# Optimization experiments

Hardware: AMD Instinct MI355X
Metric: run time of the kernel (lower is better)

Reference implementation:

```python
import jax, jax.numpy as jnp
import numpy as np

NUM_NODES = 4096
EMBED_DIM = 64
IN_DIM = 256
OUT_DIM = 256
BATCH = 32


def setup_inputs() -> dict:
    key = jax.random.key(0)
    k1, k2, k3 = jax.random.split(key, 3)
    x = jax.random.normal(k1, (BATCH, NUM_NODES, IN_DIM), dtype=jnp.float32)
    node_ids = jnp.arange(NUM_NODES, dtype=jnp.int64)
    emb_table = jax.random.normal(k2, (NUM_NODES, EMBED_DIM), dtype=jnp.float32) * 0.1
    W = jax.random.normal(k3, (IN_DIM, OUT_DIM), dtype=jnp.float32) * (1.0 / np.sqrt(IN_DIM))
    b = jnp.zeros((OUT_DIM,), dtype=jnp.float32)
    return {"x": x, "node_ids": node_ids, "emb_table": emb_table, "W": W, "b": b}


def reference(x, node_ids, emb_table, W, b):
    # Embedding lookup for node ids -> [N, E]
    E = emb_table[node_ids]
    # Adaptive adjacency from embeddings: softmax(relu(E E^T)) over neighbors
    logits = jax.nn.relu(jnp.einsum("ne,me->nm", E, E))  # [N, N]
    adj = jax.nn.softmax(logits, axis=-1)
    # Graph convolution: aggregate neighbor features, then linear + relu
    h = jnp.einsum("nm,bmd->bnd", adj, x)          # [B, N, in_dim]
    out = jax.nn.relu(jnp.einsum("bnd,do->bno", h, W) + b)  # [B, N, out_dim]
    return out
```

## Files before the change

### kernel.cpp

```cpp
#include <hip/hip_runtime.h>

#define NN   4096
#define ED   64
#define DIN  256
#define DOUT 256
#define NB   32

typedef __attribute__((ext_vector_type(8))) short bf16x8;
typedef __attribute__((ext_vector_type(4))) float f32x4;

__device__ __forceinline__ unsigned short f2bf(float f) {
    union { float f; unsigned u; } v; v.f = f;
    unsigned r = v.u + 0x7FFF + ((v.u >> 16) & 1);
    return (unsigned short)(r >> 16);
}
__device__ __forceinline__ float bf2f(unsigned short s) {
    union { unsigned u; float f; } v; v.u = ((unsigned)s) << 16;
    return v.f;
}

#define GLDS16(g, l) __builtin_amdgcn_global_load_lds( \
    (const __attribute__((address_space(1))) void*)(g), \
    (__attribute__((address_space(3))) void*)(l), 16, 0, 0)

__device__ __forceinline__ void fma4(float4& d, float s, const float4& v) {
    d.x = fmaf(s, v.x, d.x);
    d.y = fmaf(s, v.y, d.y);
    d.z = fmaf(s, v.z, d.z);
    d.w = fmaf(s, v.w, d.w);
}

__global__ void k_gather(const float* __restrict__ emb, const int* __restrict__ ids,
                         float* __restrict__ E) {
    int n = blockIdx.x;
    int e = threadIdx.x;
    int id = ids[n];
    id = id < 0 ? 0 : (id >= NN ? NN - 1 : id);
    E[(size_t)n * ED + e] = emb[(size_t)id * ED + e];
}

__global__ __launch_bounds__(256) void k_logits(const float* __restrict__ E,
                                                unsigned short* __restrict__ adjbf) {
    __shared__ __align__(16) float Ea[ED][64 + 4];
    __shared__ __align__(16) float Eb[ED][64 + 4];
    const int tid = threadIdx.x;
    const int ty = tid >> 4, tx = tid & 15;
    const int rb = blockIdx.x, cb = blockIdx.y;

    #pragma unroll
    for (int k = 0; k < 4; ++k) {
        int l = tid + k * 256;
        int row = l >> 4;
        int kq = (l & 15) * 4;
        float4 va = *(const float4*)&E[(size_t)(rb * 64 + row) * ED + kq];
        Ea[kq + 0][row] = va.x; Ea[kq + 1][row] = va.y;
        Ea[kq + 2][row] = va.z; Ea[kq + 3][row] = va.w;
        float4 vb = *(const float4*)&E[(size_t)(cb * 64 + row) * ED + kq];
        Eb[kq + 0][row] = vb.x; Eb[kq + 1][row] = vb.y;
        Eb[kq + 2][row] = vb.z; Eb[kq + 3][row] = vb.w;
    }
    __syncthreads();

    float4 acc[4] = {};
    #pragma unroll
    for (int k = 0; k < ED; ++k) {
        float4 ar = *(const float4*)&Ea[k][ty * 4];
        float4 br = *(const float4*)&Eb[k][tx * 4];
        fma4(acc[0], ar.x, br);
        fma4(acc[1], ar.y, br);
        fma4(acc[2], ar.z, br);
        fma4(acc[3], ar.w, br);
    }

    #pragma unroll
    for (int i = 0; i < 4; ++i) {
        float4 v = acc[i];
        ushort4 s;
        s.x = f2bf(fmaxf(v.x, 0.f)); s.y = f2bf(fmaxf(v.y, 0.f));
        s.z = f2bf(fmaxf(v.z, 0.f)); s.w = f2bf(fmaxf(v.w, 0.f));
        size_t n = (size_t)(rb * 64 + ty * 4 + i);
        *(ushort4*)&adjbf[n * NN + cb * 64 + tx * 4] = s;
    }
}

__global__ __launch_bounds__(256) void k_softmax(unsigned short* __restrict__ adj) {
    __shared__ float red[256];
    const int tid = threadIdx.x;
    const size_t base = (size_t)blockIdx.x * NN + (size_t)tid * 16;

    unsigned short t16[16];
    *(uint4*)&t16[0] = *(const uint4*)&adj[base];
    *(uint4*)&t16[8] = *(const uint4*)&adj[base + 8];
    float v[16];
    float mx = 0.0f;
    #pragma unroll
    for (int j = 0; j < 16; ++j) { v[j] = bf2f(t16[j]); mx = fmaxf(mx, v[j]); }

    red[tid] = mx; __syncthreads();
    for (int off = 128; off > 0; off >>= 1) {
        if (tid < off) red[tid] = fmaxf(red[tid], red[tid + off]);
        __syncthreads();
    }
    mx = red[0];
    __syncthreads();

    float s = 0.f;
    #pragma unroll
    for (int j = 0; j < 16; ++j) { v[j] = expf(v[j] - mx); s += v[j]; }
    red[tid] = s; __syncthreads();
    for (int off = 128; off > 0; off >>= 1) {
        if (tid < off) red[tid] += red[tid + off];
        __syncthreads();
    }
    const float inv = 1.0f / red[0];

    #pragma unroll
    for (int j = 0; j < 16; ++j) t16[j] = f2bf(v[j] * inv);
    *(uint4*)&adj[base]     = *(const uint4*)&t16[0];
    *(uint4*)&adj[base + 8] = *(const uint4*)&t16[8];
}

__global__ void k_wt(const float* __restrict__ W, unsigned short* __restrict__ WT) {
    int m = blockIdx.x;
    int k = threadIdx.x;
    WT[(size_t)m * DIN + k] = f2bf(W[(size_t)k * DOUT + m]);
}

__global__ __launch_bounds__(256) void k_y(const unsigned short* __restrict__ WT,
                                           const float* __restrict__ x,
                                           unsigned short* __restrict__ yT) {
    __shared__ __align__(16) short As[128 * 32];
    __shared__ __align__(16) short Bs[128 * 32];
    const int tid = threadIdx.x;
    const int lane = tid & 63, w = tid >> 6;
    const int wr = (w >> 1) * 64, wc = (w & 1) * 64;
    const int fr = lane & 15, fq = lane >> 4;
    const int m0 = blockIdx.x * 128;
    const int n0 = blockIdx.y * 128;
    const int b  = blockIdx.z;
    const float* xb = x + (size_t)b * NN * DIN;
    const int brow = tid >> 1, bh = (tid & 1) * 16;

    f32x4 acc[4][4];
    #pragma unroll
    for (int i = 0; i < 4; ++i)
        #pragma unroll
        for (int j = 0; j < 4; ++j) acc[i][j] = (f32x4){0.f, 0.f, 0.f, 0.f};

    for (int k0 = 0; k0 < DIN; k0 += 32) {
        __syncthreads();
        #pragma unroll
        for (int i = 0; i < 2; ++i) {
            int idx = (w * 2 + i) * 512 + lane * 8;
            int row = idx >> 5, kk = idx & 31;
            GLDS16(WT + (size_t)(m0 + row) * DIN + k0 + kk, &As[(w * 2 + i) * 512]);
        }
        float fv[16];
        *(float4*)&fv[0]  = *(const float4*)&xb[(size_t)(n0 + brow) * DIN + k0 + bh + 0];
        *(float4*)&fv[4]  = *(const float4*)&xb[(size_t)(n0 + brow) * DIN + k0 + bh + 4];
        *(float4*)&fv[8]  = *(const float4*)&xb[(size_t)(n0 + brow) * DIN + k0 + bh + 8];
        *(float4*)&fv[12] = *(const float4*)&xb[(size_t)(n0 + brow) * DIN + k0 + bh + 12];
        unsigned u[8];
        #pragma unroll
        for (int j = 0; j < 8; ++j)
            u[j] = (unsigned)f2bf(fv[2 * j]) | ((unsigned)f2bf(fv[2 * j + 1]) << 16);
        *(uint4*)&Bs[brow * 32 + bh]     = make_uint4(u[0], u[1], u[2], u[3]);
        *(uint4*)&Bs[brow * 32 + bh + 8] = make_uint4(u[4], u[5], u[6], u[7]);
        __syncthreads();

        bf16x8 a[4], bb[4];
        #pragma unroll
        for (int mi = 0; mi < 4; ++mi)
            a[mi] = *(const bf16x8*)&As[(wr + mi * 16 + fr) * 32 + fq * 8];
        #pragma unroll
        for (int ni = 0; ni < 4; ++ni)
            bb[ni] = *(const bf16x8*)&Bs[(wc + ni * 16 + fr) * 32 + fq * 8];
        #pragma unroll
        for (int mi = 0; mi < 4; ++mi)
            #pragma unroll
            for (int ni = 0; ni < 4; ++ni)
                acc[mi][ni] = __builtin_amdgcn_mfma_f32_16x16x32_bf16(
                    a[mi], bb[ni], acc[mi][ni], 0, 0, 0);
    }

    unsigned short* yb = yT + (size_t)b * DOUT * NN;
    #pragma unroll
    for (int mi = 0; mi < 4; ++mi)
        #pragma unroll
        for (int ni = 0; ni < 4; ++ni)
            #pragma unroll
            for (int r = 0; r < 4; ++r) {
                int row = m0 + wr + mi * 16 + fq * 4 + r;
                int col = n0 + wc + ni * 16 + fr;
                yb[(size_t)row * NN + col] = f2bf(acc[mi][ni][r]);
            }
}

__global__ __launch_bounds__(512, 2) void k_gcn(const unsigned short* __restrict__ adj,
                                                const unsigned short* __restrict__ yT,
                                                const float* __restrict__ bias,
                                                float* __restrict__ out) {
    __shared__ __align__(16) char smem[131072];

    const int tid  = threadIdx.x;
    const int lane = tid & 63, wid = tid >> 6;
    const int fr = lane & 15, fq = lane >> 4;
    const int wr = wid >> 2, wc = wid & 3;
    const int m0 = blockIdx.x * 256;
    const int by = blockIdx.y;

    const char* Apanel = (const char*)(adj + (size_t)m0 * NN);
    const char* Bpanel = (const char*)(yT + (size_t)by * DOUT * NN);

    #define STAGE4(gpan, ktb, ldsb)                                              \
        {                                                                        \
            _Pragma("unroll")                                                    \
            for (int c = 0; c < 4; ++c) {                                        \
                int bo  = c * 8192 + wid * 1024 + lane * 16;                     \
                int row = bo >> 7;                                               \
                int scol = (bo & 127) ^ ((row & 7) << 4);                        \
                GLDS16((gpan) + (size_t)row * 8192 + (ktb) + scol,               \
                       (ldsb) + c * 8192 + wid * 1024);                          \
            }                                                                    \
        }

    STAGE4(Bpanel, 0,   smem + 32768);
    STAGE4(Apanel, 0,   smem);
    STAGE4(Bpanel, 128, smem + 65536 + 32768);
    STAGE4(Apanel, 128, smem + 65536);

    f32x4 acc[8][4];
    #pragma unroll
    for (int i = 0; i < 8; ++i)
        #pragma unroll
        for (int j = 0; j < 4; ++j) acc[i][j] = (f32x4){0.f, 0.f, 0.f, 0.f};

    const int xorp0 = (fq << 4) ^ ((fr & 7) << 4);
    const int xorp1 = (64 | (fq << 4)) ^ ((fr & 7) << 4);
    const int abase = (wr * 128 + fr) * 128;
    const int bbase = (wc * 64 + fr) * 128;

    bf16x8 Ar[4][2], Br[4][2];

    for (int j = 0; j < 64; ++j) {
        const int cur = j & 1;
        char* bufA = smem + cur * 65536;
        char* bufB = bufA + 32768;

        if (j + 1 < 64) { asm volatile("s_waitcnt vmcnt(8)" ::: "memory"); }
        else            { asm volatile("s_waitcnt vmcnt(0)" ::: "memory"); }
        __builtin_amdgcn_sched_barrier(0);
        __builtin_amdgcn_s_barrier();

        #pragma unroll
        for (int mi = 0; mi < 4; ++mi) {
            Ar[mi][0] = *(const bf16x8*)(bufA + abase + mi * 2048 + xorp0);
            Ar[mi][1] = *(const bf16x8*)(bufA + abase + mi * 2048 + xorp1);
        }
        #pragma unroll
        for (int ni = 0; ni < 2; ++ni) {
            Br[ni][0] = *(const bf16x8*)(bufB + bbase + ni * 2048 + xorp0);
            Br[ni][1] = *(const bf16x8*)(bufB + bbase + ni * 2048 + xorp1);
        }
        __builtin_amdgcn_s_barrier();
        asm volatile("s_waitcnt lgkmcnt(0)" ::: "memory");
        __builtin_amdgcn_sched_barrier(0);
        __builtin_amdgcn_s_setprio(1);
        #pragma unroll
        for (int mi = 0; mi < 4; ++mi)
            #pragma unroll
            for (int ni = 0; ni < 2; ++ni) {
                acc[mi][ni] = __builtin_amdgcn_mfma_f32_16x16x32_bf16(Ar[mi][0], Br[ni][0], acc[mi][ni], 0, 0, 0);
                acc[mi][ni] = __builtin_amdgcn_mfma_f32_16x16x32_bf16(Ar[mi][1], Br[ni][1], acc[mi][ni], 0, 0, 0);
            }
        __builtin_amdgcn_s_setprio(0);
        __builtin_amdgcn_s_barrier();

        #pragma unroll
        for (int ni = 2; ni < 4; ++ni) {
            Br[ni][0] = *(const bf16x8*)(bufB + bbase + ni * 2048 + xorp0);
            Br[ni][1] = *(const bf16x8*)(bufB + bbase + ni * 2048 + xorp1);
        }
        __builtin_amdgcn_s_barrier();
        asm volatile("s_waitcnt lgkmcnt(0)" ::: "memory");
        __builtin_amdgcn_sched_barrier(0);
        __builtin_amdgcn_s_setprio(1);
        #pragma unroll
        for (int mi = 0; mi < 4; ++mi)
            #pragma unroll
            for (int ni = 2; ni < 4; ++ni) {
                acc[mi][ni] = __builtin_amdgcn_mfma_f32_16x16x32_bf16(Ar[mi][0], Br[ni][0], acc[mi][ni], 0, 0, 0);
                acc[mi][ni] = __builtin_amdgcn_mfma_f32_16x16x32_bf16(Ar[mi][1], Br[ni][1], acc[mi][ni], 0, 0, 0);
            }
        __builtin_amdgcn_s_setprio(0);
        __builtin_amdgcn_s_barrier();

        #pragma unroll
        for (int mi = 0; mi < 4; ++mi) {
            Ar[mi][0] = *(const bf16x8*)(bufA + abase + 8192 + mi * 2048 + xorp0);
            Ar[mi][1] = *(const bf16x8*)(bufA + abase + 8192 + mi * 2048 + xorp1);
        }
        if (j + 2 < 64) STAGE4(Bpanel, (j + 2) * 128, bufB);
        __builtin_amdgcn_s_barrier();
        asm volatile("s_waitcnt lgkmcnt(0)" ::: "memory");
        __builtin_amdgcn_sched_barrier(0);
        __builtin_amdgcn_s_setprio(1);
        #pragma unroll
        for (int mi = 0; mi < 4; ++mi)
            #pragma unroll
            for (int ni = 0; ni < 2; ++ni) {
                acc[4 + mi][ni] = __builtin_amdgcn_mfma_f32_16x16x32_bf16(Ar[mi][0], Br[ni][0], acc[4 + mi][ni], 0, 0, 0);
                acc[4 + mi][ni] = __builtin_amdgcn_mfma_f32_16x16x32_bf16(Ar[mi][1], Br[ni][1], acc[4 + mi][ni], 0, 0, 0);
            }
        __builtin_amdgcn_s_setprio(0);
        __builtin_amdgcn_s_barrier();

        if (j + 2 < 64) STAGE4(Apanel, (j + 2) * 128, bufA);
        __builtin_amdgcn_s_setprio(1);
        #pragma unroll
        for (int mi = 0; mi < 4; ++mi)
            #pragma unroll
            for (int ni = 2; ni < 4; ++ni) {
                acc[4 + mi][ni] = __builtin_amdgcn_mfma_f32_16x16x32_bf16(Ar[mi][0], Br[ni][0], acc[4 + mi][ni], 0, 0, 0);
                acc[4 + mi][ni] = __builtin_amdgcn_mfma_f32_16x16x32_bf16(Ar[mi][1], Br[ni][1], acc[4 + mi][ni], 0, 0, 0);
            }
        __builtin_amdgcn_s_setprio(0);
    }

    float bv[4];
    #pragma unroll
    for (int ni = 0; ni < 4; ++ni) bv[ni] = bias[wc * 64 + ni * 16 + fr];

    #pragma unroll
    for (int am = 0; am < 8; ++am) {
        const int node = m0 + wr * 128 + am * 16 + fq * 4;
        #pragma unroll
        for (int ni = 0; ni < 4; ++ni) {
            const int dcol = wc * 64 + ni * 16 + fr;
            #pragma unroll
            for (int rr = 0; rr < 4; ++rr) {
                float vv = acc[am][ni][rr] + bv[ni];
                out[((size_t)by * NN + node + rr) * DOUT + dcol] = fmaxf(vv, 0.f);
            }
        }
    }
    #undef STAGE4
}

extern "C" void kernel_launch(void* const* d_in, const int* in_sizes, int n_in,
                              void* d_out, int out_size, void* d_ws, size_t ws_size,
                              hipStream_t stream) {
    const float* x    = (const float*)d_in[0];
    const int*   ids  = (const int*)d_in[1];
    const float* emb  = (const float*)d_in[2];
    const float* W    = (const float*)d_in[3];
    const float* bias = (const float*)d_in[4];
    float* out = (float*)d_out;

    char* ws = (char*)d_ws;
    unsigned short* adjbf = (unsigned short*)ws;
    float*          E     = (float*)(ws + 33554432);
    unsigned short* WT    = (unsigned short*)(ws + 33554432 + 1048576);
    unsigned short* yT    = (unsigned short*)(ws + 33554432 + 1048576 + 131072);

    k_gather  <<<NN, ED, 0, stream>>>(emb, ids, E);
    k_logits  <<<dim3(NN / 64, NN / 64), 256, 0, stream>>>(E, adjbf);
    k_softmax <<<NN, 256, 0, stream>>>(adjbf);
    k_wt      <<<DOUT, DIN, 0, stream>>>(W, WT);
    k_y       <<<dim3(DOUT / 128, NN / 128, NB), 256, 0, stream>>>(WT, x, yT);
    k_gcn     <<<dim3(16, 32), 512, 0, stream>>>(adjbf, yT, bias, out);
}
```

Baseline: 338.8 us.

## Load full K-slice fragments once per step and collapse barrier phases

Replaces the four-phase ping-pong main loop, which interleaved LDS fragment reads, MFMA blocks, barriers and staggered global-to-LDS prefetches, with a single phase per K step. Each step now loads all A and B fragments up front, runs all 64 MFMAs, then issues both panel prefetches after one barrier. The aim is to cut barrier count and scheduling overhead. In exchange it uses more VGPRs for fragments, loses the overlap of LDS reads with MFMAs, and issues prefetches later, so global loads may be less hidden. The sched_barrier fences are also removed, which gives the compiler more freedom to reorder.

Measured after the change: 350.9 us. 1.04x slower.

```diff
diff --git a/kernel.cpp b/kernel.cpp
--- a/kernel.cpp
+++ b/kernel.cpp
@@ -240,91 +240,54 @@
     const int abase = (wr * 128 + fr) * 128;
     const int bbase = (wc * 64 + fr) * 128;
 
-    bf16x8 Ar[4][2], Br[4][2];
-
     for (int j = 0; j < 64; ++j) {
-        const int cur = j & 1;
-        char* bufA = smem + cur * 65536;
+        char* bufA = smem + (j & 1) * 65536;
         char* bufB = bufA + 32768;
 
         if (j + 1 < 64) { asm volatile("s_waitcnt vmcnt(8)" ::: "memory"); }
         else            { asm volatile("s_waitcnt vmcnt(0)" ::: "memory"); }
-        __builtin_amdgcn_sched_barrier(0);
-        __builtin_amdgcn_s_barrier();
-
-        #pragma unroll
-        for (int mi = 0; mi < 4; ++mi) {
-            Ar[mi][0] = *(const bf16x8*)(bufA + abase + mi * 2048 + xorp0);
-            Ar[mi][1] = *(const bf16x8*)(bufA + abase + mi * 2048 + xorp1);
-        }
-        #pragma unroll
-        for (int ni = 0; ni < 2; ++ni) {
+        asm volatile("s_barrier" ::: "memory");
+
+        bf16x8 Br[4][2], A0[4][2], A1[4][2];
+        #pragma unroll
+        for (int ni = 0; ni < 4; ++ni) {
             Br[ni][0] = *(const bf16x8*)(bufB + bbase + ni * 2048 + xorp0);
             Br[ni][1] = *(const bf16x8*)(bufB + bbase + ni * 2048 + xorp1);
         }
-        __builtin_amdgcn_s_barrier();
-        asm volatile("s_waitcnt lgkmcnt(0)" ::: "memory");
-        __builtin_amdgcn_sched_barrier(0);
+        #pragma unroll
+        for (int mi = 0; mi < 4; ++mi) {
+            A0[mi][0] = *(const bf16x8*)(bufA + abase + mi * 2048 + xorp0);
+            A0[mi][1] = *(const bf16x8*)(bufA + abase + mi * 2048 + xorp1);
+        }
+        #pragma unroll
+        for (int mi = 0; mi < 4; ++mi) {
+            A1[mi][0] = *(const bf16x8*)(bufA + abase + 8192 + mi * 2048 + xorp0);
+            A1[mi][1] = *(const bf16x8*)(bufA + abase + 8192 + mi * 2048 + xorp1);
+        }
+
         __builtin_amdgcn_s_setprio(1);
         #pragma unroll
         for (int mi = 0; mi < 4; ++mi)
             #pragma unroll
-            for (int ni = 0; ni < 2; ++ni) {
-                acc[mi][ni] = __builtin_amdgcn_mfma_f32_16x16x32_bf16(Ar[mi][0], Br[ni][0], acc[mi][ni], 0, 0, 0);
-                acc[mi][ni] = __builtin_amdgcn_mfma_f32_16x16x32_bf16(Ar[mi][1], Br[ni][1], acc[mi][ni], 0, 0, 0);
+            for (int ni = 0; ni < 4; ++ni) {
+                acc[mi][ni] = __builtin_amdgcn_mfma_f32_16x16x32_bf16(A0[mi][0], Br[ni][0], acc[mi][ni], 0, 0, 0);
+                acc[mi][ni] = __builtin_amdgcn_mfma_f32_16x16x32_bf16(A0[mi][1], Br[ni][1], acc[mi][ni], 0, 0, 0);
+            }
+        #pragma unroll
+        for (int mi = 0; mi < 4; ++mi)
+            #pragma unroll
+            for (int ni = 0; ni < 4; ++ni) {
+                acc[4 + mi][ni] = __builtin_amdgcn_mfma_f32_16x16x32_bf16(A1[mi][0], Br[ni][0], acc[4 + mi][ni], 0, 0, 0);
+                acc[4 + mi][ni] = __builtin_amdgcn_mfma_f32_16x16x32_bf16(A1[mi][1], Br[ni][1], acc[4 + mi][ni], 0, 0, 0);
             }
         __builtin_amdgcn_s_setprio(0);
-        __builtin_amdgcn_s_barrier();
-
-        #pragma unroll
-        for (int ni = 2; ni < 4; ++ni) {
-            Br[ni][0] = *(const bf16x8*)(bufB + bbase + ni * 2048 + xorp0);
-            Br[ni][1] = *(const bf16x8*)(bufB + bbase + ni * 2048 + xorp1);
-        }
-        __builtin_amdgcn_s_barrier();
+
         asm volatile("s_waitcnt lgkmcnt(0)" ::: "memory");
-        __builtin_amdgcn_sched_barrier(0);
-        __builtin_amdgcn_s_setprio(1);
-        #pragma unroll
-        for (int mi = 0; mi < 4; ++mi)
-            #pragma unroll
-            for (int ni = 2; ni < 4; ++ni) {
-                acc[mi][ni] = __builtin_amdgcn_mfma_f32_16x16x32_bf16(Ar[mi][0], Br[ni][0], acc[mi][ni], 0, 0, 0);
-                acc[mi][ni] = __builtin_amdgcn_mfma_f32_16x16x32_bf16(Ar[mi][1], Br[ni][1], acc[mi][ni], 0, 0, 0);
-            }
-        __builtin_amdgcn_s_setprio(0);
-        __builtin_amdgcn_s_barrier();
-
-        #pragma unroll
-        for (int mi = 0; mi < 4; ++mi) {
-            Ar[mi][0] = *(const bf16x8*)(bufA + abase + 8192 + mi * 2048 + xorp0);
-            Ar[mi][1] = *(const bf16x8*)(bufA + abase + 8192 + mi * 2048 + xorp1);
-        }
-        if (j + 2 < 64) STAGE4(Bpanel, (j + 2) * 128, bufB);
-        __builtin_amdgcn_s_barrier();
-        asm volatile("s_waitcnt lgkmcnt(0)" ::: "memory");
-        __builtin_amdgcn_sched_barrier(0);
-        __builtin_amdgcn_s_setprio(1);
-        #pragma unroll
-        for (int mi = 0; mi < 4; ++mi)
-            #pragma unroll
-            for (int ni = 0; ni < 2; ++ni) {
-                acc[4 + mi][ni] = __builtin_amdgcn_mfma_f32_16x16x32_bf16(Ar[mi][0], Br[ni][0], acc[4 + mi][ni], 0, 0, 0);
-                acc[4 + mi][ni] = __builtin_amdgcn_mfma_f32_16x16x32_bf16(Ar[mi][1], Br[ni][1], acc[4 + mi][ni], 0, 0, 0);
-            }
-        __builtin_amdgcn_s_setprio(0);
-        __builtin_amdgcn_s_barrier();
-
-        if (j + 2 < 64) STAGE4(Apanel, (j + 2) * 128, bufA);
-        __builtin_amdgcn_s_setprio(1);
-        #pragma unroll
-        for (int mi = 0; mi < 4; ++mi)
-            #pragma unroll
-            for (int ni = 2; ni < 4; ++ni) {
-                acc[4 + mi][ni] = __builtin_amdgcn_mfma_f32_16x16x32_bf16(Ar[mi][0], Br[ni][0], acc[4 + mi][ni], 0, 0, 0);
-                acc[4 + mi][ni] = __builtin_amdgcn_mfma_f32_16x16x32_bf16(Ar[mi][1], Br[ni][1], acc[4 + mi][ni], 0, 0, 0);
-            }
-        __builtin_amdgcn_s_setprio(0);
+        asm volatile("s_barrier" ::: "memory");
+        if (j + 2 < 64) {
+            STAGE4(Bpanel, (j + 2) * 128, bufB);
+            STAGE4(Apanel, (j + 2) * 128, bufA);
+        }
     }
 
     float bv[4];
```
